# Kernel tuning notes

Measured on AMD Instinct MI355X. Metric: run time of the kernel, lower is better.

Reference implementation:

```python
import jax, jax.numpy as jnp
import numpy as np

D = 2  # spatial dimension


def _conv_contract(image, filt, in_k, out_k):
    """Tensor convolution + contraction on a torus.
    image: (in_c, N, N) + (D,)*in_k
    filt:  (out_c, in_c, M, M) + (D,)*in_k + (D,)*out_k
    out:   (out_c, N, N) + (D,)*out_k
    Image tensor indices contract with the first in_k filter tensor indices.
    """
    in_c, N = image.shape[0], image.shape[1]
    out_c, M = filt.shape[0], filt.shape[2]
    di, do = D ** in_k, D ** out_k
    # fold tensor indices into channels: (1, in_c*di, N, N)
    img = jnp.transpose(image.reshape(in_c, N, N, di), (0, 3, 1, 2)).reshape(1, in_c * di, N, N)
    # filter -> (out_c*do, in_c*di, M, M), ordering (out_c, out_idx, in_c, in_idx)
    f = filt.reshape(out_c, in_c, M, M, di, do)
    f = jnp.transpose(f, (0, 5, 1, 4, 2, 3)).reshape(out_c * do, in_c * di, M, M)
    p = M // 2
    img = jnp.pad(img, ((0, 0), (0, 0), (p, p), (p, p)), mode='wrap')  # torus
    out = jax.lax.conv_general_dilated(
        img, f, window_strides=(1, 1), padding='VALID',
        dimension_numbers=('NCHW', 'OIHW', 'NCHW'))[0]
    out = jnp.transpose(out.reshape(out_c, do, N, N), (0, 2, 3, 1))
    return out.reshape((out_c, N, N) + (D,) * out_k)


def _synth(w, fils):
    # (out_c, in_c, n) x (n, M, M, tensor...) -> (out_c, in_c, M, M, tensor...)
    return jnp.einsum('oik,k...->oi...', w, fils)


def setup_inputs() -> dict:
    key = jax.random.key(0)
    ks = jax.random.split(key, 11)
    r = lambda k, s: jax.random.normal(k, s, dtype=jnp.float32)
    return {
        'x0': r(ks[0], (64, 256, 256)),
        'x1': r(ks[1], (64, 256, 256, 2)),
        'fil0': r(ks[2], (3, 3, 3)),
        'fil1': r(ks[3], (6, 3, 3, 2)),
        'fil2': r(ks[4], (12, 3, 3, 2, 2)),
        'w00': r(ks[5], (64, 64, 3)) * (1.0 / np.sqrt(64 * 3)),
        'w01': r(ks[6], (64, 64, 6)) * (1.0 / np.sqrt(64 * 6)),
        'w10': r(ks[7], (64, 64, 6)) * (1.0 / np.sqrt(64 * 6)),
        'w11': r(ks[8], (64, 64, 12)) * (1.0 / np.sqrt(64 * 12)),
        'b0': r(ks[9], (64, 1, 1)) * 0.05,
        'b1': r(ks[10], (64, 1, 1, 1)) * 0.05,
    }


def reference(x0, x1, fil0, fil1, fil2, w00, w01, w10, w11, b0, b1):
    # accumulate over input blocks for each target (out_k, out_p=0)
    out0 = _conv_contract(x0, _synth(w00, fil0), 0, 0) \
         + _conv_contract(x1, _synth(w10, fil1), 1, 0)
    out1 = _conv_contract(x0, _synth(w01, fil1), 0, 1) \
         + _conv_contract(x1, _synth(w11, fil2), 1, 1)
    # use_bias='auto': plain bias for scalars, mean-scaled bias for tensors
    out0 = out0 + b0
    mean1 = jnp.mean(out1, axis=(1, 2), keepdims=True)  # spatial mean
    out1 = out1 + mean1 * b1
    return (out0, out1)
```

## Files before the change

kernel.cpp:

```cpp
#include <hip/hip_runtime.h>
#include <hip/hip_bf16.h>
#include <string.h>


#define NN 256
#define NPIX 65536
#define OUT1_OFF 4194304
#define XB_CH 4096
#define FG_C 30720
#define XTILE 24576

typedef __attribute__((ext_vector_type(8))) short short8;
typedef __attribute__((ext_vector_type(4))) float floatx4;

__device__ __forceinline__ unsigned short f2b(float x) {
    unsigned int u; memcpy(&u, &x, 4);
    return (unsigned short)((u + 0x7FFFu + ((u >> 16) & 1u)) >> 16);
}
__device__ __forceinline__ float b2f16(unsigned short u) {
    unsigned int v = ((unsigned int)u) << 16; float f; memcpy(&f, &v, 4); return f;
}
__device__ __forceinline__ unsigned int pack2(float a, float b) {
    return (unsigned int)f2b(a) | ((unsigned int)f2b(b) << 16);
}

__global__ __launch_bounds__(256) void prep_kernel(const float* __restrict__ x0,
                                                   const float* __restrict__ x1,
                                                   unsigned short* __restrict__ Xb,
                                                   float* __restrict__ partial) {
    const int t = threadIdx.x;
    const int w = t >> 6, tx = t & 63;
    const int bxs = blockIdx.x;
    const int yg = ((bxs & 7) << 3) | (bxs >> 3);
    const int y = yg * 4 + w;
    const int c = blockIdx.y;
    const int col0 = tx * 4;

    unsigned int u[4][8];
    float sum[16];
    if (c < 4) {
        #pragma unroll
        for (int j = 0; j < 8; j++) {
            const float4 a = *(const float4*)(x0 + (size_t)(16 * c + 2 * j) * NPIX + y * NN + col0);
            const float4 b = *(const float4*)(x0 + (size_t)(16 * c + 2 * j + 1) * NPIX + y * NN + col0);
            u[0][j] = pack2(a.x, b.x);
            u[1][j] = pack2(a.y, b.y);
            u[2][j] = pack2(a.z, b.z);
            u[3][j] = pack2(a.w, b.w);
            sum[2 * j]     = a.x + a.y + a.z + a.w;
            sum[2 * j + 1] = b.x + b.y + b.z + b.w;
        }
    } else {
        #pragma unroll
        for (int j = 0; j < 8; j++) {
            int i = 8 * (c - 4) + j;
            const float* base = x1 + ((size_t)(i * 256 + y) * 256 + col0) * 2;
            const float4 p0 = *(const float4*)(base);
            const float4 p1 = *(const float4*)(base + 4);
            u[0][j] = pack2(p0.x, p0.y);
            u[1][j] = pack2(p0.z, p0.w);
            u[2][j] = pack2(p1.x, p1.y);
            u[3][j] = pack2(p1.z, p1.w);
            sum[2 * j]     = p0.x + p0.z + p1.x + p1.z;
            sum[2 * j + 1] = p0.y + p0.w + p1.y + p1.w;
        }
    }
    char* rowp = (char*)(Xb + ((size_t)y * 12 + c) * XB_CH);
    #pragma unroll
    for (int cc = 0; cc < 4; cc++) {
        int col = col0 + cc;
        int sw = ((col >> 3) & 7) << 4;
        *(uint4*)(rowp + ((col * 32)      ^ sw)) = make_uint4(u[cc][0], u[cc][1], u[cc][2], u[cc][3]);
        *(uint4*)(rowp + ((col * 32 + 16) ^ sw)) = make_uint4(u[cc][4], u[cc][5], u[cc][6], u[cc][7]);
    }
    #pragma unroll
    for (int cl = 0; cl < 16; cl++)
        #pragma unroll
        for (int d = 1; d < 64; d <<= 1) sum[cl] += __shfl_xor(sum[cl], d, 64);
    if (tx < 16) partial[(c * 16 + tx) * 256 + y] = sum[tx];
}

__global__ void synth_kernel(const float* __restrict__ fil0, const float* __restrict__ fil1,
                             const float* __restrict__ fil2,
                             const float* __restrict__ w00, const float* __restrict__ w01,
                             const float* __restrict__ w10, const float* __restrict__ w11,
                             unsigned short* __restrict__ Fg) {
    int idx = blockIdx.x * 256 + threadIdx.x;
    if (idx >= 12 * 12 * 5 * 512) return;
    int sub = idx & 511;
    int blk = idx >> 9;
    int ks = blk % 5;
    int rc = blk / 5;
    int rt = rc % 12;
    int c = rc / 12;
    int lane = sub >> 3, j = sub & 7;
    int quad = lane >> 4, ln = lane & 15;
    int co = rt * 16 + ln;
    int kpos = ks * 32 + quad * 8 + j;
    int tap = kpos >> 4, cl = kpos & 15;
    float s = 0.0f;
    if (tap < 9) {
        int cin = c * 16 + cl;
        if (co < 64) {
            if (cin < 64) {
                for (int k = 0; k < 3; k++)
                    s += w00[(co * 64 + cin) * 3 + k] * fil0[k * 9 + tap];
            } else {
                int i = (cin - 64) >> 1, t = (cin - 64) & 1;
                for (int k = 0; k < 6; k++)
                    s += w10[(co * 64 + i) * 6 + k] * fil1[(k * 9 + tap) * 2 + t];
            }
        } else {
            int o = (co - 64) >> 1, u = (co - 64) & 1;
            if (cin < 64) {
                for (int k = 0; k < 6; k++)
                    s += w01[(o * 64 + cin) * 6 + k] * fil1[(k * 9 + tap) * 2 + u];
            } else {
                int i = (cin - 64) >> 1, t = (cin - 64) & 1;
                for (int k = 0; k < 12; k++)
                    s += w11[(o * 64 + i) * 12 + k] * fil2[((k * 9 + tap) * 2 + t) * 2 + u];
            }
        }
    }
    Fg[idx] = f2b(s);
}

__global__ void meanbx_kernel(const unsigned short* __restrict__ Fg,
                              const float* __restrict__ partial,
                              const float* __restrict__ b1, float* __restrict__ meanb) {
    __shared__ float mX[192];
    __shared__ float rd[4];
    const int c1 = blockIdx.x;
    const int t = threadIdx.x;
    if (t < 192) {
        const float4* p = (const float4*)(partial + (size_t)t * 256);
        float s = 0.0f;
        for (int j = 0; j < 64; j++) { float4 v = p[j]; s += v.x + v.y + v.z + v.w; }
        mX[t] = s * (1.0f / 65536.0f);
    }
    __syncthreads();
    float s = 0.0f;
    for (int e = t; e < 1728; e += 256) {
        int c = e / 144, r = e - c * 144;
        int cl = r & 15;
        int fidx = ((c * 12 + 4 + (c1 >> 4)) * 5 + (r >> 5)) * 512
                 + ((((r >> 3) & 3) * 16 + (c1 & 15)) << 3) + (r & 7);
        s += b2f16(Fg[fidx]) * mX[c * 16 + cl];
    }
#pragma unroll
    for (int d = 1; d < 64; d <<= 1) s += __shfl_xor(s, d, 64);
    if ((t & 63) == 0) rd[t >> 6] = s;
    __syncthreads();
    if (t == 0) meanb[c1] = (rd[0] + rd[1] + rd[2] + rd[3]) * b1[c1 >> 1];
}

__global__ __launch_bounds__(512, 4) void conv_kernel(
    const unsigned short* __restrict__ Xb, const unsigned short* __restrict__ Fg,
    const float* __restrict__ b0, const float* __restrict__ meanb,
    float* __restrict__ out) {

    __shared__ __align__(16) char lds[2 * XTILE];

    const int tid = threadIdx.x;
    const int bx = blockIdx.x;
    const int y = ((bx & 7) << 5) | (bx >> 3);
    const int m0 = blockIdx.y * 96;
    const int l = tid & 63, w = tid >> 6;
    const int wm = w >> 2, wn = w & 3;
    const int nw = wn * 64;
    const int ln = l & 15, quad = l >> 4;

    const unsigned short* pF[3];
#pragma unroll
    for (int f = 0; f < 3; f++) {
        int rt = blockIdx.y * 6 + wm * 3 + f;
        pF[f] = Fg + ((size_t)rt * 320 + l) * 8;
    }

    int addrB[5][4];
#pragma unroll
    for (int ks = 0; ks < 5; ks++) {
        int tap = 2 * ks + (quad >> 1);
        int r, dx;
        if (tap > 8) { r = 0; dx = 0; }
        else { r = tap / 3; dx = tap - 3 * r - 1; }
#pragma unroll
        for (int g = 0; g < 4; g++) {
            int colw = (nw + g * 16 + ln + dx) & 255;
            addrB[ks][g] = r * 8192 +
                ((colw * 32 + (quad & 1) * 16) ^ (((colw >> 3) & 7) << 4));
        }
    }

    floatx4 acc[3][4];
#pragma unroll
    for (int f = 0; f < 3; f++)
#pragma unroll
        for (int g = 0; g < 4; g++) acc[f][g] = (floatx4){0.f, 0.f, 0.f, 0.f};

    auto stage = [&](int c, int bsel) {
        char* base = lds + bsel * XTILE;
#pragma unroll
        for (int i = 0; i < 3; i++) {
            int yr = (y + i + 255) & 255;
            const unsigned short* g = Xb + ((size_t)yr * 12 + c) * XB_CH + w * 512;
            __builtin_amdgcn_global_load_lds(
                (const __attribute__((address_space(1))) unsigned int*)(g + l * 8),
                (__attribute__((address_space(3))) unsigned int*)(base + i * 8192 + w * 1024),
                16, 0, 0);
        }
    };

    stage(0, 0);
    __syncthreads();

    int cur = 0;
    size_t coff = 0;
    for (int c = 0; c < 12; c++) {
        if (c < 11) stage(c + 1, cur ^ 1);
        const char* xb = lds + cur * XTILE;
#pragma unroll
        for (int ks = 0; ks < 5; ks++) {
            short8 A[3], B[4];
#pragma unroll
            for (int f = 0; f < 3; f++)
                A[f] = *(const short8*)(pF[f] + coff + ks * 512);
#pragma unroll
            for (int g = 0; g < 4; g++)
                B[g] = *(const short8*)(xb + addrB[ks][g]);
#pragma unroll
            for (int f = 0; f < 3; f++)
#pragma unroll
                for (int g = 0; g < 4; g++)
                    acc[f][g] = __builtin_amdgcn_mfma_f32_16x16x32_bf16(A[f], B[g], acc[f][g], 0, 0, 0);
        }
        coff += FG_C;
        __syncthreads();
        cur ^= 1;
    }

    const int mw = wm * 48;
#pragma unroll
    for (int f = 0; f < 3; f++) {
        int cob = m0 + mw + f * 16 + quad * 4;
#pragma unroll
        for (int g = 0; g < 4; g++) {
            int col = nw + g * 16 + ln;
            if (cob < 64) {
#pragma unroll
                for (int reg = 0; reg < 4; reg++)
                    out[(size_t)(cob + reg) * NPIX + y * NN + col] = acc[f][g][reg] + b0[cob + reg];
            } else {
#pragma unroll
                for (int reg = 0; reg < 4; reg += 2) {
                    int c1 = cob + reg - 64;
                    int o = c1 >> 1;
                    float2 v = make_float2(acc[f][g][reg] + meanb[c1],
                                           acc[f][g][reg + 1] + meanb[c1 + 1]);
                    *((float2*)(out + OUT1_OFF) + ((size_t)o * NPIX + y * NN + col)) = v;
                }
            }
        }
    }
}

extern "C" void kernel_launch(void* const* d_in, const int* in_sizes, int n_in,
                              void* d_out, int out_size, void* d_ws, size_t ws_size,
                              hipStream_t stream) {
    const float* x0   = (const float*)d_in[0];
    const float* x1   = (const float*)d_in[1];
    const float* fil0 = (const float*)d_in[2];
    const float* fil1 = (const float*)d_in[3];
    const float* fil2 = (const float*)d_in[4];
    const float* w00  = (const float*)d_in[5];
    const float* w01  = (const float*)d_in[6];
    const float* w10  = (const float*)d_in[7];
    const float* w11  = (const float*)d_in[8];
    const float* b0   = (const float*)d_in[9];
    const float* b1   = (const float*)d_in[10];

    unsigned short* Xb = (unsigned short*)d_ws;
    unsigned short* Fg = (unsigned short*)((char*)d_ws + 25165824);
    float* partial     = (float*)((char*)d_ws + 25903104);
    float* meanb       = (float*)((char*)d_ws + 26099712);
    float* out = (float*)d_out;

    prep_kernel<<<dim3(64, 12), 256, 0, stream>>>(x0, x1, Xb, partial);

    synth_kernel<<<(12 * 12 * 5 * 512 + 255) / 256, 256, 0, stream>>>(
        fil0, fil1, fil2, w00, w01, w10, w11, Fg);

    meanbx_kernel<<<128, 256, 0, stream>>>(Fg, partial, b1, meanb);

    conv_kernel<<<dim3(NN, 2), 512, 0, stream>>>(Xb, Fg, b0, meanb, out);
}
```

Baseline: 184.1 us.

## Switch conv to 32x32x16 MFMA with all output channels per block and LDS-staged filters

```diff
diff --git a/kernel.cpp b/kernel.cpp
--- a/kernel.cpp
+++ b/kernel.cpp
@@ -7,11 +7,13 @@
 #define NPIX 65536
 #define OUT1_OFF 4194304
 #define XB_CH 4096
-#define FG_C 30720
-#define XTILE 24576
+#define FG_C 27648
+#define FBYT 55296
+#define XOFF 55296
+#define BUFB 79872
 
 typedef __attribute__((ext_vector_type(8))) short short8;
-typedef __attribute__((ext_vector_type(4))) float floatx4;
+typedef __attribute__((ext_vector_type(16))) float floatx16;
 
 __device__ __forceinline__ unsigned short f2b(float x) {
     unsigned int u; memcpy(&u, &x, 4);
@@ -69,7 +71,7 @@
     #pragma unroll
     for (int cc = 0; cc < 4; cc++) {
         int col = col0 + cc;
-        int sw = ((col >> 3) & 7) << 4;
+        int sw = (col & 7) << 4;
         *(uint4*)(rowp + ((col * 32)      ^ sw)) = make_uint4(u[cc][0], u[cc][1], u[cc][2], u[cc][3]);
         *(uint4*)(rowp + ((col * 32 + 16) ^ sw)) = make_uint4(u[cc][4], u[cc][5], u[cc][6], u[cc][7]);
     }
@@ -86,20 +88,13 @@
                              const float* __restrict__ w10, const float* __restrict__ w11,
                              unsigned short* __restrict__ Fg) {
     int idx = blockIdx.x * 256 + threadIdx.x;
-    if (idx >= 12 * 12 * 5 * 512) return;
-    int sub = idx & 511;
-    int blk = idx >> 9;
-    int ks = blk % 5;
-    int rc = blk / 5;
-    int rt = rc % 12;
-    int c = rc / 12;
-    int lane = sub >> 3, j = sub & 7;
-    int quad = lane >> 4, ln = lane & 15;
-    int co = rt * 16 + ln;
-    int kpos = ks * 32 + quad * 8 + j;
+    if (idx >= 12 * 192 * 144) return;
+    int kpos = idx % 144;
+    int co   = (idx / 144) % 192;
+    int c    = idx / (144 * 192);
     int tap = kpos >> 4, cl = kpos & 15;
     float s = 0.0f;
-    if (tap < 9) {
+    {
         int cin = c * 16 + cl;
         if (co < 64) {
             if (cin < 64) {
@@ -122,7 +117,9 @@
             }
         }
     }
-    Fg[idx] = f2b(s);
+    int swz = (tap < 8) ? ((co & 7) << 3) : (((co >> 2) & 1) << 3);
+    int off = ((tap * 16 + (cl & 8)) ^ swz) + (cl & 7);
+    Fg[((size_t)c * 192 + co) * 144 + off] = f2b(s);
 }
 
 __global__ void meanbx_kernel(const unsigned short* __restrict__ Fg,
@@ -142,10 +139,10 @@
     float s = 0.0f;
     for (int e = t; e < 1728; e += 256) {
         int c = e / 144, r = e - c * 144;
-        int cl = r & 15;
-        int fidx = ((c * 12 + 4 + (c1 >> 4)) * 5 + (r >> 5)) * 512
-                 + ((((r >> 3) & 3) * 16 + (c1 & 15)) << 3) + (r & 7);
-        s += b2f16(Fg[fidx]) * mX[c * 16 + cl];
+        int tap = r >> 4, cl = r & 15;
+        int swz = (tap < 8) ? ((c1 & 7) << 3) : (((c1 >> 2) & 1) << 3);
+        int off = ((tap * 16 + (cl & 8)) ^ swz) + (cl & 7);
+        s += b2f16(Fg[((size_t)c * 192 + 64 + c1) * 144 + off]) * mX[c * 16 + cl];
     }
 #pragma unroll
     for (int d = 1; d < 64; d <<= 1) s += __shfl_xor(s, d, 64);
@@ -154,60 +151,66 @@
     if (t == 0) meanb[c1] = (rd[0] + rd[1] + rd[2] + rd[3]) * b1[c1 >> 1];
 }
 
-__global__ __launch_bounds__(512, 4) void conv_kernel(
+__global__ __launch_bounds__(512, 2) void conv_kernel(
     const unsigned short* __restrict__ Xb, const unsigned short* __restrict__ Fg,
     const float* __restrict__ b0, const float* __restrict__ meanb,
     float* __restrict__ out) {
 
-    __shared__ __align__(16) char lds[2 * XTILE];
+    __shared__ __align__(16) char lds[2 * BUFB];
 
     const int tid = threadIdx.x;
     const int bx = blockIdx.x;
     const int y = ((bx & 7) << 5) | (bx >> 3);
-    const int m0 = blockIdx.y * 96;
     const int l = tid & 63, w = tid >> 6;
     const int wm = w >> 2, wn = w & 3;
     const int nw = wn * 64;
-    const int ln = l & 15, quad = l >> 4;
-
-    const unsigned short* pF[3];
-#pragma unroll
-    for (int f = 0; f < 3; f++) {
-        int rt = blockIdx.y * 6 + wm * 3 + f;
-        pF[f] = Fg + ((size_t)rt * 320 + l) * 8;
-    }
-
-    int addrB[5][4];
-#pragma unroll
-    for (int ks = 0; ks < 5; ks++) {
-        int tap = 2 * ks + (quad >> 1);
-        int r, dx;
-        if (tap > 8) { r = 0; dx = 0; }
-        else { r = tap / 3; dx = tap - 3 * r - 1; }
-#pragma unroll
-        for (int g = 0; g < 4; g++) {
-            int colw = (nw + g * 16 + ln + dx) & 255;
-            addrB[ks][g] = r * 8192 +
-                ((colw * 32 + (quad & 1) * 16) ^ (((colw >> 3) & 7) << 4));
-        }
-    }
-
-    floatx4 acc[3][4];
+    const int l31 = l & 31;
+    const int hi16 = (l >> 5) << 4;
+    const int swzA = (l & 7) << 4;
+    const int swzA8 = (l & 4) << 2;
+
+    int rowterm[3];
 #pragma unroll
     for (int f = 0; f < 3; f++)
-#pragma unroll
-        for (int g = 0; g < 4; g++) acc[f][g] = (floatx4){0.f, 0.f, 0.f, 0.f};
+        rowterm[f] = (wm * 96 + f * 32 + l31) * 288;
+
+    int addrB[9][2];
+#pragma unroll
+    for (int t = 0; t < 9; t++) {
+        int r = t / 3, dx = t % 3 - 1;
+#pragma unroll
+        for (int g = 0; g < 2; g++) {
+            int colw = (nw + g * 32 + l31 + dx) & 255;
+            addrB[t][g] = XOFF + r * 8192 + ((colw * 32 + hi16) ^ ((colw & 7) << 4));
+        }
+    }
+
+    floatx16 acc[3][2];
+#pragma unroll
+    for (int f = 0; f < 3; f++)
+#pragma unroll
+        for (int g = 0; g < 2; g++)
+#pragma unroll
+            for (int r = 0; r < 16; r++) acc[f][g][r] = 0.f;
 
     auto stage = [&](int c, int bsel) {
-        char* base = lds + bsel * XTILE;
-#pragma unroll
-        for (int i = 0; i < 3; i++) {
-            int yr = (y + i + 255) & 255;
-            const unsigned short* g = Xb + ((size_t)yr * 12 + c) * XB_CH + w * 512;
+        char* base = lds + bsel * BUFB;
+        for (int s = w; s < 78; s += 8) {
+            const unsigned short* g;
+            char* lb;
+            if (s < 54) {
+                g = Fg + (size_t)c * FG_C + s * 512;
+                lb = base + s * 1024;
+            } else {
+                int j = s - 54;
+                int r = j >> 3, p = j & 7;
+                int yr = (y + r + 255) & 255;
+                g = Xb + ((size_t)yr * 12 + c) * XB_CH + p * 512;
+                lb = base + XOFF + r * 8192 + p * 1024;
+            }
             __builtin_amdgcn_global_load_lds(
                 (const __attribute__((address_space(1))) unsigned int*)(g + l * 8),
-                (__attribute__((address_space(3))) unsigned int*)(base + i * 8192 + w * 1024),
-                16, 0, 0);
+                (__attribute__((address_space(3))) unsigned int*)lb, 16, 0, 0);
         }
     };
 
@@ -215,49 +218,52 @@
     __syncthreads();
 
     int cur = 0;
-    size_t coff = 0;
     for (int c = 0; c < 12; c++) {
         if (c < 11) stage(c + 1, cur ^ 1);
-        const char* xb = lds + cur * XTILE;
-#pragma unroll
-        for (int ks = 0; ks < 5; ks++) {
-            short8 A[3], B[4];
+        const char* fb = lds + cur * BUFB;
+#pragma unroll
+        for (int t = 0; t < 9; t++) {
+            short8 A[3], B[2];
+            int kterm = (t < 8) ? ((t * 32 + hi16) ^ swzA)
+                                : ((256 + hi16) ^ swzA8);
 #pragma unroll
             for (int f = 0; f < 3; f++)
-                A[f] = *(const short8*)(pF[f] + coff + ks * 512);
-#pragma unroll
-            for (int g = 0; g < 4; g++)
-                B[g] = *(const short8*)(xb + addrB[ks][g]);
+                A[f] = *(const short8*)(fb + rowterm[f] + kterm);
+#pragma unroll
+            for (int g = 0; g < 2; g++)
+                B[g] = *(const short8*)(fb + addrB[t][g]);
 #pragma unroll
             for (int f = 0; f < 3; f++)
 #pragma unroll
-                for (int g = 0; g < 4; g++)
-                    acc[f][g] = __builtin_amdgcn_mfma_f32_16x16x32_bf16(A[f], B[g], acc[f][g], 0, 0, 0);
-        }
-        coff += FG_C;
+                for (int g = 0; g < 2; g++)
+                    acc[f][g] = __builtin_amdgcn_mfma_f32_32x32x16_bf16(A[f], B[g], acc[f][g], 0, 0, 0);
+        }
         __syncthreads();
         cur ^= 1;
     }
 
-    const int mw = wm * 48;
+    const int hi4 = (l >> 5) * 4;
 #pragma unroll
     for (int f = 0; f < 3; f++) {
-        int cob = m0 + mw + f * 16 + quad * 4;
-#pragma unroll
-        for (int g = 0; g < 4; g++) {
-            int col = nw + g * 16 + ln;
-            if (cob < 64) {
-#pragma unroll
-                for (int reg = 0; reg < 4; reg++)
-                    out[(size_t)(cob + reg) * NPIX + y * NN + col] = acc[f][g][reg] + b0[cob + reg];
-            } else {
-#pragma unroll
-                for (int reg = 0; reg < 4; reg += 2) {
-                    int c1 = cob + reg - 64;
-                    int o = c1 >> 1;
-                    float2 v = make_float2(acc[f][g][reg] + meanb[c1],
-                                           acc[f][g][reg + 1] + meanb[c1 + 1]);
-                    *((float2*)(out + OUT1_OFF) + ((size_t)o * NPIX + y * NN + col)) = v;
+#pragma unroll
+        for (int g = 0; g < 2; g++) {
+            int col = nw + g * 32 + l31;
+#pragma unroll
+            for (int rr = 0; rr < 4; rr++) {
+                int co0 = wm * 96 + f * 32 + hi4 + 8 * rr;
+                if (co0 < 64) {
+#pragma unroll
+                    for (int q = 0; q < 4; q++)
+                        out[(size_t)(co0 + q) * NPIX + y * NN + col] =
+                            acc[f][g][rr * 4 + q] + b0[co0 + q];
+                } else {
+#pragma unroll
+                    for (int q = 0; q < 4; q += 2) {
+                        int c1 = co0 + q - 64;
+                        float2 v = make_float2(acc[f][g][rr * 4 + q] + meanb[c1],
+                                               acc[f][g][rr * 4 + q + 1] + meanb[c1 + 1]);
+                        *((float2*)(out + OUT1_OFF) + ((size_t)(c1 >> 1) * NPIX + y * NN + col)) = v;
+                    }
                 }
             }
         }
@@ -281,16 +287,16 @@
 
     unsigned short* Xb = (unsigned short*)d_ws;
     unsigned short* Fg = (unsigned short*)((char*)d_ws + 25165824);
-    float* partial     = (float*)((char*)d_ws + 25903104);
-    float* meanb       = (float*)((char*)d_ws + 26099712);
+    float* partial     = (float*)((char*)d_ws + 25829376);
+    float* meanb       = (float*)((char*)d_ws + 26025984);
     float* out = (float*)d_out;
 
     prep_kernel<<<dim3(64, 12), 256, 0, stream>>>(x0, x1, Xb, partial);
 
-    synth_kernel<<<(12 * 12 * 5 * 512 + 255) / 256, 256, 0, stream>>>(
+    synth_kernel<<<(12 * 192 * 144 + 255) / 256, 256, 0, stream>>>(
         fil0, fil1, fil2, w00, w01, w10, w11, Fg);
 
     meanbx_kernel<<<128, 256, 0, stream>>>(Fg, partial, b1, meanb);
 
-    conv_kernel<<<dim3(NN, 2), 512, 0, stream>>>(Xb, Fg, b0, meanb, out);
-}
+    conv_kernel<<<dim3(256), 512, 0, stream>>>(Xb, Fg, b0, meanb, out);
+}
```

Result: faster. 174.3 us (-5.3%).
